# Kernel tuning notes

Hardware: AMD Instinct MI355X
Metric: run time of the kernel (lower is better)

Reference implementation:

```python
import jax, jax.numpy as jnp
import numpy as np
import math

E = 3        # e_layers
D = 512      # d_model
H = 8        # n_heads
FACTOR = 5
NEG = -1e9   # large-negative stand-in for -inf causal mask (same softmax result, NaN-safe)


def _layernorm(x, g, b, eps=1e-5):
    mu = jnp.mean(x, -1, keepdims=True)
    xc = x - mu
    var = jnp.mean(xc * xc, -1, keepdims=True)
    return g * xc * jax.lax.rsqrt(var + eps) + b


def _conv1d(x, w, b, pad):
    # x: [B,C,L], w: [O,I,K]
    y = jax.lax.conv_general_dilated(x, w, (1,), [pad], dimension_numbers=('NCH', 'OIH', 'NCH'))
    return y + b[None, :, None]


def _maxpool3s2(x):
    # x: [B,C,L] -> kernel 3, stride 2, pad 1
    return jax.lax.reduce_window(x, -jnp.inf, jax.lax.max, (1, 1, 3), (1, 1, 2), [(0, 0), (0, 0), (1, 1)])


def _prob_sparse(h, mask, wq, bq, wk, bk, wv, bv, wo, bo, key):
    B, L, Dm = h.shape
    hd = Dm // H
    scale = hd ** -0.5
    split = lambda y: y.reshape(B, L, H, hd).transpose(0, 2, 1, 3)  # [B,H,L,hd]
    Q = split(h @ wq + bq)
    K = split(h @ wk + bk)
    V = split(h @ wv + bv)
    U = FACTOR * int(math.ceil(math.log(L)))
    u = min(U, L)
    sample_k = min(U, L)
    perm = jax.random.permutation(key, L)[:sample_k]
    K_sample = K[:, :, perm, :]                                     # [B,H,sk,hd]
    qks = jnp.einsum('bhld,bhsd->bhls', Q, K_sample) * scale        # [B,H,L,sk]
    M = qks.max(-1) - qks.mean(-1)                                  # sparsity measure [B,H,L]
    _, idx = jax.lax.top_k(M, u)                                    # [B,H,u]
    Q_reduce = jnp.take_along_axis(Q, idx[..., None], axis=2)       # [B,H,u,hd]
    logits = jnp.einsum('bhud,bhld->bhul', Q_reduce, K) * scale + mask[idx]  # [B,H,u,L]
    attn = jax.nn.softmax(logits, -1)
    out_reduce = jnp.einsum('bhul,bhld->bhud', attn, V)             # [B,H,u,hd]
    out = jnp.broadcast_to(V.mean(axis=2, keepdims=True), (B, H, L, hd))
    out = out.at[jnp.arange(B)[:, None, None], jnp.arange(H)[None, :, None], idx].set(out_reduce)
    return out.transpose(0, 2, 1, 3).reshape(B, L, Dm) @ wo + bo


def setup_inputs() -> dict:
    key = jax.random.key(0)
    it = iter(jax.random.split(key, 64))
    nrm = lambda *sh: jax.random.normal(next(it), sh, jnp.float32) * 0.02
    B, L, IN = 8, 4096, 64
    inp = {}
    inp['x'] = jax.random.normal(next(it), (B, L, IN), jnp.float32)
    inp['time_features'] = jax.random.normal(next(it), (B, L, 2), jnp.float32)
    inp['in_w'] = nrm(IN, D)
    inp['in_b'] = jnp.zeros((D,), jnp.float32)
    inp['pos_emb'] = nrm(1, L, D)
    inp['tp_w'] = nrm(2, D)
    inp['tp_b'] = jnp.zeros((D,), jnp.float32)
    inp['pos_scale'] = jnp.ones((1,), jnp.float32)
    inp['temporal_scale'] = jnp.ones((1,), jnp.float32)
    inp['conv_w'] = nrm(E, D, D, 3)
    inp['conv_b'] = jnp.zeros((E, D), jnp.float32)
    for nm in ('wq', 'wk', 'wv', 'wo'):
        inp[nm] = nrm(E, D, D)
    for nm in ('bq', 'bk', 'bv', 'bo'):
        inp[nm] = jnp.zeros((E, D), jnp.float32)
    inp['f1_w'] = nrm(E, D, 4 * D)
    inp['f1_b'] = jnp.zeros((E, 4 * D), jnp.float32)
    inp['f2_w'] = nrm(E, 4 * D, D)
    inp['f2_b'] = jnp.zeros((E, D), jnp.float32)
    for nm in ('g1', 'g2', 'g3'):
        inp[nm] = jnp.ones((E, D), jnp.float32)
    for nm in ('be1', 'be2', 'be3'):
        inp[nm] = jnp.zeros((E, D), jnp.float32)
    inp['dconv_w'] = nrm(E - 1, D, D, 3)
    inp['dconv_b'] = jnp.zeros((E - 1, D), jnp.float32)
    return inp


def reference(x, time_features, in_w, in_b, pos_emb, tp_w, tp_b, pos_scale, temporal_scale,
              conv_w, conv_b, wq, bq, wk, bk, wv, bv, wo, bo,
              f1_w, f1_b, f2_w, f2_b, g1, be1, g2, be2, g3, be3, dconv_w, dconv_b):
    B, L, _ = x.shape
    h = x @ in_w + in_b + pos_scale * pos_emb[:, :L] + temporal_scale * (time_features @ tp_w + tp_b)
    for i in range(E):
        Lc = h.shape[1]
        mask = jnp.triu(jnp.full((Lc, Lc), NEG, h.dtype), k=1)
        # causal conv: left-pad 2, kernel 3
        c = _conv1d(h.transpose(0, 2, 1), conv_w[i], conv_b[i], (2, 0)).transpose(0, 2, 1)
        h = _layernorm(h + c, g1[i], be1[i])
        a = _prob_sparse(h, mask, wq[i], bq[i], wk[i], bk[i], wv[i], bv[i], wo[i], bo[i],
                         jax.random.fold_in(jax.random.key(42), i))
        h = _layernorm(h + a, g2[i], be2[i])
        f = jax.nn.relu(h @ f1_w[i] + f1_b[i]) @ f2_w[i] + f2_b[i]
        h = _layernorm(h + f, g3[i], be3[i])
        if i < E - 1:
            hc = _conv1d(h.transpose(0, 2, 1), dconv_w[i], dconv_b[i], (1, 1))
            h = _maxpool3s2(jax.nn.elu(hc)).transpose(0, 2, 1)
    return h
```

## Files before the change

kernel.cpp:

```cpp
#include <hip/hip_runtime.h>
#include <cstdint>
#include <cmath>
#include <cstddef>

#define DD 512
#define NEGV -1000000000.0f
#define MAXU 45

typedef unsigned short ushort_t;
typedef __attribute__((ext_vector_type(8))) short short8v;
typedef __attribute__((ext_vector_type(4))) float float4v;

__device__ __forceinline__ ushort_t bfbits(float x) {
  uint32_t u = __float_as_uint(x);
  return (ushort_t)((u + 0x7FFFu + ((u >> 16) & 1u)) >> 16);
}
__device__ __forceinline__ float bfval(ushort_t b) {
  return __uint_as_float(((uint32_t)b) << 16);
}
__device__ __forceinline__ void split3(float x, ushort_t& o0, ushort_t& o1, ushort_t& o2) {
  ushort_t b0 = bfbits(x); float f0 = bfval(b0);
  float r1 = x - f0;       ushort_t b1 = bfbits(r1); float f1 = bfval(b1);
  float r2 = r1 - f1;      o2 = bfbits(r2);
  o0 = b0; o1 = b1;
}

__device__ __forceinline__ void d_tf(uint32_t k0, uint32_t k1,
                                     uint32_t c0, uint32_t c1,
                                     uint32_t& o0, uint32_t& o1) {
  const uint32_t ks2 = k0 ^ k1 ^ 0x1BD11BDAu;
  uint32_t v0 = c0 + k0, v1 = c1 + k1;
#define RR(r) { v0 += v1; v1 = (v1 << r) | (v1 >> (32 - r)); v1 ^= v0; }
  RR(13) RR(15) RR(26) RR(6)  v0 += k1;  v1 += ks2 + 1u;
  RR(17) RR(29) RR(16) RR(24) v0 += ks2; v1 += k0 + 2u;
  RR(13) RR(15) RR(26) RR(6)  v0 += k0;  v1 += k1 + 3u;
  RR(17) RR(29) RR(16) RR(24) v0 += k1;  v1 += ks2 + 4u;
  RR(13) RR(15) RR(26) RR(6)  v0 += ks2; v1 += k0 + 5u;
#undef RR
  o0 = v0; o1 = v1;
}

__device__ __forceinline__ uint32_t bits_elem(int B, uint32_t k0, uint32_t k1,
                                              uint32_t i, uint32_t total) {
  uint32_t a, b;
  switch (B) {
    case 0: case 1: {
      const uint32_t half = total >> 1;
      if (i < half) { d_tf(k0, k1, i, i + half, a, b); return B == 0 ? a : b; }
      d_tf(k0, k1, i - half, i, a, b); return B == 0 ? b : a;
    }
    case 2: d_tf(k0, k1, 0u, i, a, b); return a;
    case 3: d_tf(k0, k1, 0u, i, a, b); return b;
    case 4: d_tf(k0, k1, 0u, i, a, b); return a ^ b;
    case 5: d_tf(k0, k1, i, 0u, a, b); return a;
    case 6: d_tf(k0, k1, i, 0u, a, b); return b;
    default: d_tf(k0, k1, i, 0u, a, b); return a ^ b;
  }
}

__device__ __forceinline__ void split_row2(int S, int B, uint32_t k0, uint32_t k1,
                                           int num, int row,
                                           uint32_t& o0, uint32_t& o1) {
  uint32_t a, b;
  switch (S) {
    case 0: case 2: {
      const bool sw = (S == 2);
      const int m0 = 2 * row, m1 = 2 * row + 1;
      if (m0 < num) { d_tf(k0, k1, (uint32_t)m0, (uint32_t)(m0 + num), a, b); o0 = sw ? b : a; }
      else          { d_tf(k0, k1, (uint32_t)(m0 - num), (uint32_t)m0, a, b); o0 = sw ? a : b; }
      if (m1 < num) { d_tf(k0, k1, (uint32_t)m1, (uint32_t)(m1 + num), a, b); o1 = sw ? b : a; }
      else          { d_tf(k0, k1, (uint32_t)(m1 - num), (uint32_t)m1, a, b); o1 = sw ? a : b; }
      return;
    }
    case 1: {
      if (B >= 5) d_tf(k0, k1, (uint32_t)row, 0u, o0, o1);
      else        d_tf(k0, k1, 0u, (uint32_t)row, o0, o1);
      return;
    }
    default: {
      const uint32_t p0 = 2 * row, p1 = 2 * row + 1;
      uint32_t x0, x1, y0, y1;
      if (B >= 5) { d_tf(k0, k1, p0, 0u, x0, x1); d_tf(k0, k1, p1, 0u, y0, y1); }
      else        { d_tf(k0, k1, 0u, p0, x0, x1); d_tf(k0, k1, 0u, p1, y0, y1); }
      if (S == 3)      { o0 = x0;      o1 = y0; }
      else if (S == 4) { o0 = x1;      o1 = y1; }
      else             { o0 = x0 ^ x1; o1 = y0 ^ y1; }
      return;
    }
  }
}

__global__ __launch_bounds__(64) void probe_k(const float* __restrict__ x,
                                              int* __restrict__ flag) {
  const int t = threadIdx.x;
  const float val_ref = erff(x[t] * 0.70710678118654752f);
  const float lo = __uint_as_float(0xBF7FFFFFu);
  const float span = 1.0f - lo;
  int match = -1;
  for (int S = 0; S < 6; ++S) {
    for (int B = 0; B < 8; ++B) {
      uint32_t xk0, xk1;
      split_row2(S, B, 0u, 0u, 64, 0, xk0, xk1);
      const uint32_t bits = bits_elem(B, xk0, xk1, (uint32_t)t, 1u << 21);
      const float u = __uint_as_float((bits >> 9) | 0x3F800000u) - 1.0f;
      const float val = fmaxf(lo, u * span + lo);
      const unsigned long long m = __ballot(fabsf(val - val_ref) < 2e-2f);
      if (match < 0 && __popcll(m) >= 58) match = S * 8 + B;
    }
  }
  uint32_t s00, s01, s10, s11;
  split_row2(0, 0, 0u, 0u, 2, 0, s00, s01);
  split_row2(0, 0, 0u, 0u, 2, 1, s10, s11);
  const int self_ok = (s00 == 4146024105u && s01 == 967050713u &&
                       s10 == 2718843009u && s11 == 1272950319u) ? 1 : 0;
  if (t == 0) { flag[0] = match; flag[1] = self_ok; }
}

__global__ __launch_bounds__(1024) void perm_k(const int* __restrict__ flag,
                                               int* __restrict__ permout,
                                               int L, int U, int layer) {
  __shared__ unsigned long long comp[4096];
  __shared__ int xs[4096];
  const int tid = threadIdx.x;
  int c = flag[0]; if (c < 0) c = 0;
  const int S = c >> 3, B = c & 7;
  uint32_t k0, k1;
  d_tf(0u, 42u, 0u, (uint32_t)layer, k0, k1);
  const int rounds = (L >= 2048) ? 2 : 1;
  for (int i = tid; i < L; i += 1024) xs[i] = i;
  __syncthreads();
  for (int r = 0; r < rounds; ++r) {
    uint32_t nk0, nk1, sk0, sk1;
    split_row2(S, B, k0, k1, 2, 0, nk0, nk1);
    split_row2(S, B, k0, k1, 2, 1, sk0, sk1);
    k0 = nk0; k1 = nk1;
    for (int i = tid; i < L; i += 1024) {
      const uint32_t bits = bits_elem(B, sk0, sk1, (uint32_t)i, (uint32_t)L);
      comp[i] = ((unsigned long long)bits << 32) | (unsigned)i;
    }
    __syncthreads();
    for (int kk = 2; kk <= L; kk <<= 1) {
      for (int jj = kk >> 1; jj > 0; jj >>= 1) {
        for (int t2 = tid; t2 < (L >> 1); t2 += 1024) {
          const int i = ((t2 & ~(jj - 1)) << 1) | (t2 & (jj - 1));
          const int ixj = i | jj;
          const bool asc = ((i & kk) == 0);
          const unsigned long long a = comp[i], b = comp[ixj];
          if ((a > b) == asc) { comp[i] = b; comp[ixj] = a; }
        }
        __syncthreads();
      }
    }
    int vals[4]; int n = 0;
    for (int i = tid; i < L; i += 1024) vals[n++] = xs[comp[i] & 0xFFFFFFFFu];
    __syncthreads();
    n = 0;
    for (int i = tid; i < L; i += 1024) xs[i] = vals[n++];
    __syncthreads();
  }
  for (int i = tid; i < U; i += 1024) permout[i] = xs[i];
}

__global__ void diag_k(const int* __restrict__ flag, float* __restrict__ out) {
  if (threadIdx.x == 0 && blockIdx.x == 0 && flag[0] < 0)
    out[0] = flag[1] ? 54321.0f : 94321.0f;
}

__global__ void zero_pads_k(ushort_t* __restrict__ A0, ushort_t* __restrict__ A1,
                            ushort_t* __restrict__ A2, int PR, int total) {
  const int i = blockIdx.x * 256 + threadIdx.x;
  if (i >= total) return;
  const int bl = i / 1536;
  const int rem = i - bl * 1536;
  const int pj = rem >> 9, c = rem & 511;
  const int j = (pj < 2) ? pj : (PR - 1);
  const size_t o = ((size_t)bl * PR + j) * 512 + c;
  A0[o] = 0; A1[o] = 0; A2[o] = 0;
}

__global__ __launch_bounds__(256) void embed_split_k(
    const float* __restrict__ x, const float* __restrict__ tfe,
    const float* __restrict__ in_w, const float* __restrict__ in_b,
    const float* __restrict__ pos_emb, const float* __restrict__ tp_w,
    const float* __restrict__ tp_b, const float* __restrict__ ps,
    const float* __restrict__ ts, ushort_t* __restrict__ A0,
    ushort_t* __restrict__ A1, ushort_t* __restrict__ A2,
    int L, int lcs, int PR) {
  const int r = blockIdx.x;
  const int l = r & (L - 1);
  const int bl = r >> lcs;
  __shared__ float xs[64];
  __shared__ float tfs[2];
  const int t = threadIdx.x;
  if (t < 64) xs[t] = x[(size_t)r * 64 + t];
  if (t < 2)  tfs[t] = tfe[(size_t)r * 2 + t];
  __syncthreads();
  const float p = ps[0], tsc = ts[0];
  const size_t ob = ((size_t)bl * PR + 2 + l) * 512;
  for (int c = t; c < DD; c += 256) {
    float s = in_b[c];
#pragma unroll 8
    for (int k = 0; k < 64; ++k) s = fmaf(xs[k], in_w[k * DD + c], s);
    float tv = tfs[0] * tp_w[c] + tfs[1] * tp_w[DD + c] + tp_b[c];
    const float v = s + p * pos_emb[(size_t)l * DD + c] + tsc * tv;
    ushort_t u0, u1, u2; split3(v, u0, u1, u2);
    A0[ob + c] = u0; A1[ob + c] = u1; A2[ob + c] = u2;
  }
}

__global__ void wsplit_k(const float* __restrict__ W, ushort_t* __restrict__ B0,
                         ushort_t* __restrict__ B1, ushort_t* __restrict__ B2,
                         int K, int N, int conv, int total) {
  const int i = blockIdx.x * 256 + threadIdx.x;
  if (i >= total) return;
  const int n = i / K, k = i - n * K;
  const float v = conv ? W[(size_t)n * 1536 + (k & 511) * 3 + (k >> 9)]
                       : W[(size_t)k * N + n];
  ushort_t u0, u1, u2; split3(v, u0, u1, u2);
  B0[i] = u0; B1[i] = u1; B2[i] = u2;
}

__global__ void cat2_k(const float* __restrict__ a, const float* __restrict__ b,
                       float* __restrict__ o) {
  const int i = blockIdx.x * 256 + threadIdx.x;
  if (i < 512) o[i] = a[i];
  else if (i < 1024) o[i] = b[i - 512];
}

__global__ void asm_split_k(const int* __restrict__ map, const float* __restrict__ outred,
                            const float* __restrict__ vm, ushort_t* __restrict__ A0,
                            ushort_t* __restrict__ A1, ushort_t* __restrict__ A2,
                            int U, int Lc, int lcs, int PR, int bc, long total) {
  const long i = (long)blockIdx.x * 256 + threadIdx.x;
  if (i >= total) return;
  const int c = (int)(i & 511);
  const long r = i >> 9;
  const int bl = (int)(r >> lcs);
  const int t = (int)(r & (Lc - 1));
  const int b = bc + bl;
  const int head = c >> 6, d = c & 63;
  const int bh = b * 8 + head;
  const int j = map[(size_t)bh * Lc + t];
  const float v = (j >= 0) ? outred[((size_t)(bh * U + j) << 6) + d]
                           : vm[(bh << 6) + d];
  ushort_t u0, u1, u2; split3(v, u0, u1, u2);
  const size_t o = ((size_t)bl * PR + 2 + t) * 512 + c;
  A0[o] = u0; A1[o] = u1; A2[o] = u2;
}

template <int MH, int NW>
__global__ __launch_bounds__(256, (MH + NW <= 2) ? 4 : ((MH == 1) ? 4 : 3))
void gemm6_k(
    const ushort_t* __restrict__ A0, const ushort_t* __restrict__ A1,
    const ushort_t* __restrict__ A2, const ushort_t* __restrict__ B0,
    const ushort_t* __restrict__ B1, const ushort_t* __restrict__ B2,
    float* __restrict__ C, float* __restrict__ C2,
    ushort_t* __restrict__ Co0, ushort_t* __restrict__ Co1,
    ushort_t* __restrict__ Co2, const float* __restrict__ bias,
    int N, int K, int RS, int PR, int Foff, int lcs, int rowoff, int relu,
    int mode, int conv3, int p3) {
  __shared__ ushort_t sm[6144 * MH + 6144 * NW];
  const int tid = threadIdx.x;
  const int nwg = gridDim.x * gridDim.y;
  const int bid0 = blockIdx.y * gridDim.x + blockIdx.x;
  const int wgid = ((bid0 & 7) * (nwg >> 3)) + (bid0 >> 3);
  const int bn = (wgid % gridDim.x) * (64 * NW);
  const int bm = (wgid / gridDim.x) * (64 * MH);
  const int lane = tid & 63;
  const int w = tid >> 6;
  const int wn = w * (16 * NW);
  const int l15 = lane & 15;
  const int c16r = lane >> 4;
  const int Lcm = (1 << lcs) - 1;
  float4v acc[MH][4][NW] = {};

  const int NCH = 3 * MH + 3 * NW;
  const ushort_t* gp[NCH];
  int lb[NCH];
  int isl2[NCH];
  {
    const int rowc = lane >> 2;
    const int slot = lane & 3;
#pragma unroll
    for (int j = 0; j < NCH; ++j) {
      const int q = w + 4 * j;
      if (q < 12 * MH) {
        const int limb = q / (4 * MH), ql = q % (4 * MH);
        const int rl = ql * 16 + rowc;
        const int dcol = slot ^ ((rl >> 1) & 3);
        const int r = rowoff + bm + rl;
        const int b = r >> lcs, t = r & Lcm;
        const size_t off = ((size_t)(b * PR + Foff + t)) * RS + dcol * 8;
        gp[j] = (limb == 0 ? A0 : limb == 1 ? A1 : A2) + off;
        isl2[j] = (limb == 2);
      } else {
        const int qq = q - 12 * MH;
        const int limb = qq / (4 * NW), ql = qq % (4 * NW);
        const int rl = ql * 16 + rowc;
        const int dcol = slot ^ ((rl >> 1) & 3);
        const size_t off = ((size_t)(bn + rl)) * K + dcol * 8;
        gp[j] = (limb == 0 ? B0 : limb == 1 ? B1 : B2) + off;
        isl2[j] = (limb == 2);
      }
      lb[j] = q * 512;
    }
  }

  const int ABASE1 = 2048 * MH, ABASE2 = 4096 * MH;
  const int BBASE = 6144 * MH;
  const int BL = 2048 * NW;
  const int nsteps = K >> 5;
  for (int s = 0; s < nsteps; ++s) {
    const int k0 = conv3 ? ((s % 3) * 512 + (s / 3) * 32) : (s * 32);
#pragma unroll
    for (int j = 0; j < NCH; ++j) {
      if (p3 && isl2[j]) continue;
      __builtin_amdgcn_global_load_lds(
          (const __attribute__((address_space(1))) void*)(gp[j] + k0),
          (__attribute__((address_space(3))) void*)(sm + lb[j]),
          16, 0, 0);
    }
    __syncthreads();
    short8v bg0[NW], bg1[NW], bg2[NW];
#pragma unroll
    for (int g = 0; g < NW; ++g) {
      const int r = wn + g * 16 + l15;
      const int br = r * 32 + ((c16r ^ ((r >> 1) & 3)) << 3);
      bg0[g] = *(const short8v*)(sm + BBASE + br);
      bg1[g] = *(const short8v*)(sm + BBASE + BL + br);
      if (!p3) bg2[g] = *(const short8v*)(sm + BBASE + 2 * BL + br);
    }
#pragma unroll
    for (int h = 0; h < MH; ++h) {
#pragma unroll
      for (int mf = 0; mf < 4; ++mf) {
        const int r = h * 64 + mf * 16 + l15;
        const int ar = r * 32 + ((c16r ^ ((r >> 1) & 3)) << 3);
        const short8v a0 = *(const short8v*)(sm + ar);
        const short8v a1 = *(const short8v*)(sm + ABASE1 + ar);
#pragma unroll
        for (int nf = 0; nf < NW; ++nf) {
          float4v c = acc[h][mf][nf];
          c = __builtin_amdgcn_mfma_f32_16x16x32_bf16(a0, bg0[nf], c, 0, 0, 0);
          c = __builtin_amdgcn_mfma_f32_16x16x32_bf16(a0, bg1[nf], c, 0, 0, 0);
          c = __builtin_amdgcn_mfma_f32_16x16x32_bf16(a1, bg0[nf], c, 0, 0, 0);
          acc[h][mf][nf] = c;
        }
        if (!p3) {
          const short8v a2 = *(const short8v*)(sm + ABASE2 + ar);
#pragma unroll
          for (int nf = 0; nf < NW; ++nf) {
            float4v c = acc[h][mf][nf];
            c = __builtin_amdgcn_mfma_f32_16x16x32_bf16(a1, bg1[nf], c, 0, 0, 0);
            c = __builtin_amdgcn_mfma_f32_16x16x32_bf16(a0, bg2[nf], c, 0, 0, 0);
            c = __builtin_amdgcn_mfma_f32_16x16x32_bf16(a2, bg0[nf], c, 0, 0, 0);
            acc[h][mf][nf] = c;
          }
        }
      }
    }
    __syncthreads();
  }
  const int cbase = bn + wn + l15;
#pragma unroll
  for (int h = 0; h < MH; ++h) {
    const int rbase = bm + h * 64 + ((lane >> 4) << 2);
#pragma unroll
    for (int mf = 0; mf < 4; ++mf)
#pragma unroll
      for (int nf = 0; nf < NW; ++nf)
#pragma unroll
        for (int j = 0; j < 4; ++j) {
          const int row = rbase + mf * 16 + j;
          const int col = cbase + nf * 16;
          float v = acc[h][mf][nf][j] + bias[col];
          if (relu) v = fmaxf(v, 0.f);
          if (mode == 0) {
            C[(size_t)row * N + col] = v;
          } else if (mode == 1) {
            ushort_t u0, u1, u2; split3(v, u0, u1, u2);
            const size_t o = (size_t)row * N + col;
            Co0[o] = u0; Co1[o] = u1; Co2[o] = u2;
          } else {
            float* dst = (col >> 9) ? C2 : C;
            dst[(size_t)row * 512 + (col & 511)] = v;
          }
        }
  }
}

__global__ __launch_bounds__(64) void resid_ln_split_k(
    const ushort_t* __restrict__ A0, const ushort_t* __restrict__ A1,
    const ushort_t* __restrict__ A2, const float* __restrict__ res,
    const float* __restrict__ g, const float* __restrict__ be,
    ushort_t* __restrict__ O0, ushort_t* __restrict__ O1,
    ushort_t* __restrict__ O2, float* __restrict__ fout,
    int Lc, int lcs, int PR, int final_out) {
  const int r = blockIdx.x;
  const int t = threadIdx.x;
  const size_t lbase = (((size_t)(r >> lcs)) * PR + 2 + (r & (Lc - 1))) * 512 + t * 8;
  const short8v l0 = *(const short8v*)(A0 + lbase);
  const short8v l1 = *(const short8v*)(A1 + lbase);
  const short8v l2 = *(const short8v*)(A2 + lbase);
  const float4* rp = (const float4*)(res + (size_t)r * DD + t * 8);
  const float4 r0 = rp[0], r1 = rp[1];
  float h[8];
#pragma unroll
  for (int j = 0; j < 8; ++j)
    h[j] = bfval((ushort_t)l0[j]) + bfval((ushort_t)l1[j]) + bfval((ushort_t)l2[j]);
  h[0] += r0.x; h[1] += r0.y; h[2] += r0.z; h[3] += r0.w;
  h[4] += r1.x; h[5] += r1.y; h[6] += r1.z; h[7] += r1.w;
  float s = 0.f, q = 0.f;
#pragma unroll
  for (int j = 0; j < 8; ++j) { s += h[j]; q += h[j] * h[j]; }
  for (int off = 32; off; off >>= 1) { s += __shfl_down(s, off); q += __shfl_down(q, off); }
  s = __shfl(s, 0); q = __shfl(q, 0);
  const float mu = s * (1.f / 512.f);
  const float var = q * (1.f / 512.f) - mu * mu;
  const float rs = rsqrtf(var + 1e-5f);
  const int c0 = t * 8;
  if (final_out) {
    float o[8];
#pragma unroll
    for (int j = 0; j < 8; ++j)
      o[j] = g[c0 + j] * (h[j] - mu) * rs + be[c0 + j];
    float4* op = (float4*)(fout + (size_t)r * DD + c0);
    op[0] = make_float4(o[0], o[1], o[2], o[3]);
    op[1] = make_float4(o[4], o[5], o[6], o[7]);
  } else {
    short8v o0, o1v, o2;
#pragma unroll
    for (int j = 0; j < 8; ++j) {
      const float v = g[c0 + j] * (h[j] - mu) * rs + be[c0 + j];
      ushort_t u0, u1, u2; split3(v, u0, u1, u2);
      o0[j] = (short)u0; o1v[j] = (short)u1; o2[j] = (short)u2;
    }
    *(short8v*)(O0 + lbase) = o0;
    *(short8v*)(O1 + lbase) = o1v;
    *(short8v*)(O2 + lbase) = o2;
  }
}

__global__ __launch_bounds__(256) void sample_m3_k(
    const float* __restrict__ Q, const float* __restrict__ Kb,
    float* __restrict__ Mv, const int* __restrict__ perm,
    int U, int Lc, int lcs) {
  const int tile = blockIdx.x;
  const int bh = blockIdx.y;
  const int head = bh & 7, b = bh >> 3;
  const int t = threadIdx.x;
  __shared__ float ks[MAXU][65];
  for (int e = t; e < U * 64; e += 256) {
    const int j = e >> 6, d = e & 63;
    ks[j][d] = Kb[(((size_t)b << lcs) + perm[j]) * DD + head * 64 + d];
  }
  __syncthreads();
  const int l = tile * 256 + t;
  const float4* qr = (const float4*)(Q + (((size_t)b << lcs) + l) * DD + head * 64);
  float q[64];
#pragma unroll
  for (int d4 = 0; d4 < 16; ++d4) {
    const float4 v = qr[d4];
    q[d4 * 4] = v.x; q[d4 * 4 + 1] = v.y; q[d4 * 4 + 2] = v.z; q[d4 * 4 + 3] = v.w;
  }
  float smax = -1e30f, ssum = 0.f;
  for (int j = 0; j < U; ++j) {
    float s = 0.f;
#pragma unroll
    for (int d = 0; d < 64; ++d) s = fmaf(q[d], ks[j][d], s);
    smax = fmaxf(smax, s); ssum += s;
  }
  Mv[(size_t)bh * Lc + l] = 0.125f * (smax - ssum / (float)U);
}

__global__ __launch_bounds__(256) void topk_k(
    const float* __restrict__ Mv, int* __restrict__ idx, int Lc, int U) {
  __shared__ float mv[4096];
  __shared__ float rv[256];
  __shared__ int ri[256];
  const int bh = blockIdx.x;
  const int t = threadIdx.x;
  const float* Mp = Mv + (size_t)bh * Lc;
  for (int i = t; i < Lc; i += 256) mv[i] = Mp[i];
  __syncthreads();
  for (int j = 0; j < U; ++j) {
    float best = -INFINITY; int bi = 0x7fffffff;
    for (int i = t; i < Lc; i += 256) {
      const float v = mv[i];
      if (v > best) { best = v; bi = i; }
    }
    rv[t] = best; ri[t] = bi;
    __syncthreads();
    for (int s2 = 128; s2; s2 >>= 1) {
      if (t < s2) {
        if (rv[t + s2] > rv[t] || (rv[t + s2] == rv[t] && ri[t + s2] < ri[t])) {
          rv[t] = rv[t + s2]; ri[t] = ri[t + s2];
        }
      }
      __syncthreads();
    }
    if (t == 0) { idx[bh * U + j] = ri[0]; mv[ri[0]] = -INFINITY; }
    __syncthreads();
  }
}

__global__ void gather_q_k(const float* __restrict__ Q, const int* __restrict__ idx,
                           float* __restrict__ Qsel, int U, int Lc, int lc_shift,
                           int total) {
  const int i = blockIdx.x * 256 + threadIdx.x;
  if (i >= total) return;
  const int d = i & 63;
  const int gj = i >> 6;
  const int bh = gj / U;
  const int head = bh & 7, b = bh >> 3;
  const int qi = idx[gj];
  Qsel[i] = Q[(((size_t)b << lc_shift) + qi) * DD + head * 64 + d];
}

__global__ __launch_bounds__(256, 4) void attn_flash_k(
    const float* __restrict__ Qsel, const float* __restrict__ Kb,
    const float* __restrict__ V, const int* __restrict__ idx,
    float* __restrict__ Oseg, float* __restrict__ mseg, float* __restrict__ lseg,
    int U, int Lc, int lcs, int SEG) {
  const int seg = blockIdx.x;
  const int bh = blockIdx.y;
  const int head = bh & 7, b = bh >> 3;
  const int t = threadIdx.x;
  __shared__ float q[48][65];
  __shared__ float kt[32][65];
  __shared__ float vt[32][65];
  __shared__ float ps[48][33];
  __shared__ float mArr[48], lArr[48], fArr[48];
  __shared__ int qiArr[48];
  __shared__ int qmaxs;
#pragma unroll
  for (int i = 0; i < 12; ++i) {
    const int e = i * 256 + t;
    q[e >> 6][e & 63] = (e < U * 64) ? Qsel[(size_t)bh * U * 64 + e] : 0.f;
  }
  if (t < 48) {
    qiArr[t] = (t < U) ? idx[bh * U + t] : -1;
    mArr[t] = -1e30f; lArr[t] = 0.f; fArr[t] = 1.f;
  }
  if (t == 0) {
    int qm = 0;
    for (int j = 0; j < U; ++j) qm = max(qm, idx[bh * U + j]);
    qmaxs = qm;
  }
  float acc[12];
#pragma unroll
  for (int i = 0; i < 12; ++i) acc[i] = 0.f;
  __syncthreads();
  const int segl = Lc / SEG;
  const int s0 = seg * segl, s1 = s0 + segl;
  const int qmax = qmaxs;
  const size_t kvbase = ((size_t)b << lcs) * DD + head * 64;
  for (int t0 = s0; t0 < s1; t0 += 32) {
    if (t0 > qmax) break;
#pragma unroll
    for (int i = 0; i < 2; ++i) {
      const int idx4 = t + 256 * i;
      const int r = idx4 >> 4;
      const int c4 = (idx4 & 15) << 2;
      const float4 kv = *(const float4*)(Kb + kvbase + (size_t)(t0 + r) * DD + c4);
      const float4 vv = *(const float4*)(V + kvbase + (size_t)(t0 + r) * DD + c4);
      kt[r][c4] = kv.x; kt[r][c4 + 1] = kv.y; kt[r][c4 + 2] = kv.z; kt[r][c4 + 3] = kv.w;
      vt[r][c4] = vv.x; vt[r][c4 + 1] = vv.y; vt[r][c4 + 2] = vv.z; vt[r][c4 + 3] = vv.w;
    }
    __syncthreads();
#pragma unroll
    for (int i = 0; i < 6; ++i) {
      const int pair = i * 256 + t;
      const int qq = pair >> 5, l = pair & 31;
      const float* qr = q[qq];
      const float* kr = kt[l];
      float s = 0.f;
#pragma unroll
      for (int d = 0; d < 64; ++d) s = fmaf(qr[d], kr[d], s);
      s *= 0.125f;
      if (t0 + l > qiArr[qq]) s = NEGV;
      ps[qq][l] = s;
    }
    __syncthreads();
    if (t < U) {
      float mrow = -1e30f;
      for (int l = 0; l < 32; ++l) mrow = fmaxf(mrow, ps[t][l]);
      const float mnew = fmaxf(mArr[t], mrow);
      const float f = expf(mArr[t] - mnew);
      float sum = 0.f;
      for (int l = 0; l < 32; ++l) {
        const float e = expf(ps[t][l] - mnew);
        ps[t][l] = e; sum += e;
      }
      lArr[t] = lArr[t] * f + sum;
      mArr[t] = mnew; fArr[t] = f;
    }
    __syncthreads();
#pragma unroll
    for (int i = 0; i < 12; ++i) {
      const int pair = i * 256 + t;
      const int qq = pair >> 6, d = pair & 63;
      float a = acc[i] * fArr[qq];
      const float* pr = ps[qq];
#pragma unroll
      for (int l = 0; l < 32; ++l) a = fmaf(pr[l], vt[l][d], a);
      acc[i] = a;
    }
    __syncthreads();
  }
  const size_t obase = ((size_t)(bh * SEG + seg)) * U * 64;
#pragma unroll
  for (int i = 0; i < 12; ++i) {
    const int pair = i * 256 + t;
    if (pair < U * 64) Oseg[obase + pair] = acc[i];
  }
  if (t < U) {
    mseg[(bh * SEG + seg) * U + t] = mArr[t];
    lseg[(bh * SEG + seg) * U + t] = lArr[t];
  }
}

__global__ void attn_comb_k(const float* __restrict__ Oseg,
                            const float* __restrict__ mseg,
                            const float* __restrict__ lseg,
                            float* __restrict__ outred, int U, int SEG) {
  const int bh = blockIdx.x;
  const int t = threadIdx.x;
  for (int i = 0; i < 12; ++i) {
    const int pair = i * 256 + t;
    if (pair >= U * 64) break;
    const int qq = pair >> 6;
    float m = -1e30f;
    for (int s = 0; s < SEG; ++s) m = fmaxf(m, mseg[(bh * SEG + s) * U + qq]);
    float l = 0.f, o = 0.f;
    for (int s = 0; s < SEG; ++s) {
      const float w = expf(mseg[(bh * SEG + s) * U + qq] - m);
      l += w * lseg[(bh * SEG + s) * U + qq];
      o += w * Oseg[((size_t)(bh * SEG + s)) * U * 64 + pair];
    }
    outred[(size_t)bh * U * 64 + pair] = o / l;
  }
}

__global__ __launch_bounds__(256) void vmean1_k(
    const float* __restrict__ V, float* __restrict__ vpart, int Lc, int lcs) {
  const int seg = blockIdx.x;
  const int bh = blockIdx.y;
  const int head = bh & 7, b = bh >> 3;
  const int t = threadIdx.x;
  const int d = t & 63, c = t >> 6;
  const int segl = Lc >> 4;
  const int l0 = seg * segl;
  float s = 0.f;
  for (int l = l0 + c; l < l0 + segl; l += 4)
    s += V[(((size_t)b << lcs) + l) * DD + head * 64 + d];
  __shared__ float red[256];
  red[t] = s; __syncthreads();
  if (t < 64)
    vpart[((bh * 16 + seg) << 6) + t] = red[t] + red[64 + t] + red[128 + t] + red[192 + t];
}

__global__ void vmean2_k(const float* __restrict__ vpart, float* __restrict__ vm,
                         int Lc) {
  const int bh = blockIdx.x;
  const int d = threadIdx.x;
  float s = 0.f;
  for (int seg = 0; seg < 16; ++seg) s += vpart[((bh * 16 + seg) << 6) + d];
  vm[(bh << 6) + d] = s / (float)Lc;
}

__global__ void fill_i32_k(int* __restrict__ p, int n, int v) {
  const int i = blockIdx.x * 256 + threadIdx.x;
  if (i < n) p[i] = v;
}

__global__ void scatter_k(const int* __restrict__ idx, int* __restrict__ map,
                          int U, int Lc, int total) {
  const int i = blockIdx.x * 256 + threadIdx.x;
  if (i < total) map[(size_t)(i / U) * Lc + idx[i]] = i % U;
}

__global__ void elu_pool_split_k(const float* __restrict__ X,
                                 ushort_t* __restrict__ A0, ushort_t* __restrict__ A1,
                                 ushort_t* __restrict__ A2,
                                 int Lc, int lcs, int PRn, long total) {
  const long i = (long)blockIdx.x * 256 + threadIdx.x;
  if (i >= total) return;
  const int c = (int)(i & 511);
  const long r = i >> 9;
  const int half = Lc >> 1;
  const int t2 = (int)(r & (half - 1));
  const int bl = (int)(r >> (lcs - 1));
  float m = -INFINITY;
  const int t00 = 2 * t2 - 1;
  for (int dt = 0; dt < 3; ++dt) {
    const int tt = t00 + dt;
    if (tt >= 0 && tt < Lc) {
      float v = X[(((size_t)bl << lcs) + tt) * 512 + c];
      v = v > 0.f ? v : expm1f(v);
      m = fmaxf(m, v);
    }
  }
  ushort_t u0, u1, u2; split3(m, u0, u1, u2);
  const size_t o = ((size_t)bl * PRn + 2 + t2) * 512 + c;
  A0[o] = u0; A1[o] = u1; A2[o] = u2;
}

extern "C" void kernel_launch(void* const* d_in, const int* in_sizes, int n_in,
                              void* d_out, int out_size, void* d_ws, size_t ws_size,
                              hipStream_t stream) {
  (void)in_sizes; (void)n_in; (void)out_size;
  const float* x       = (const float*)d_in[0];
  const float* tfe     = (const float*)d_in[1];
  const float* in_w    = (const float*)d_in[2];
  const float* in_b    = (const float*)d_in[3];
  const float* pos_emb = (const float*)d_in[4];
  const float* tp_w    = (const float*)d_in[5];
  const float* tp_b    = (const float*)d_in[6];
  const float* pos_s   = (const float*)d_in[7];
  const float* tmp_s   = (const float*)d_in[8];
  const float* conv_w  = (const float*)d_in[9];
  const float* conv_b  = (const float*)d_in[10];
  const float* wq      = (const float*)d_in[11];
  const float* wk      = (const float*)d_in[12];
  const float* wv      = (const float*)d_in[13];
  const float* wo      = (const float*)d_in[14];
  const float* bq      = (const float*)d_in[15];
  const float* bk      = (const float*)d_in[16];
  const float* bv      = (const float*)d_in[17];
  const float* bo      = (const float*)d_in[18];
  const float* f1_w    = (const float*)d_in[19];
  const float* f1_b    = (const float*)d_in[20];
  const float* f2_w    = (const float*)d_in[21];
  const float* f2_b    = (const float*)d_in[22];
  const float* g1      = (const float*)d_in[23];
  const float* g2      = (const float*)d_in[24];
  const float* g3      = (const float*)d_in[25];
  const float* be1     = (const float*)d_in[26];
  const float* be2     = (const float*)d_in[27];
  const float* be3     = (const float*)d_in[28];
  const float* dconv_w = (const float*)d_in[29];
  const float* dconv_b = (const float*)d_in[30];

  const size_t SZ = 16777216;
  const size_t HSF = 16789504;
  const size_t WSZ = 1048576;
  const size_t CSZ = 8400896;
  float* ws    = (float*)d_ws;
  float* slotB = ws;
  float* slotC = ws + SZ;
  ushort_t* hA0 = (ushort_t*)(ws + 2 * SZ);
  ushort_t* hA1 = hA0 + HSF;
  ushort_t* hA2 = hA1 + HSF;
  ushort_t* w10 = hA2 + HSF; ushort_t* w11 = w10 + WSZ; ushort_t* w12 = w11 + WSZ;
  ushort_t* w20 = w12 + WSZ; ushort_t* w21 = w20 + WSZ; ushort_t* w22 = w21 + WSZ;
  float* Mb    = (float*)(w22 + WSZ);
  float* ORb   = Mb + 262144;
  float* VMb   = ORb + 196608;
  int*   idxb  = (int*)(VMb + 8192);
  int*   mapb  = idxb + 8192;
  int*   flagb = mapb + 262144;
  int*   permb = flagb + 64;
  float* Qselb = (float*)(permb + 64);
  float* bcatb = Qselb + 196608;
  float* vpartb = bcatb + 1024;
  float* Osegb = vpartb + 65536;
  float* msegb = Osegb + 2949120;
  float* lsegb = msegb + 46080;
  const size_t NEED = (size_t)((char*)(lsegb + 46080) - (char*)ws);
  if (ws_size < NEED) return;

  ushort_t* cs0 = (ushort_t*)slotC;
  ushort_t* cs1 = cs0 + CSZ;
  ushort_t* cs2 = cs1 + CSZ;
  ushort_t* fc0 = (ushort_t*)slotC;
  ushort_t* fc1 = fc0 + (size_t)4096 * 2048;
  ushort_t* fc2 = fc1 + (size_t)4096 * 2048;

  probe_k<<<1, 64, 0, stream>>>(x, flagb);

  int L = 4096;
  {
    int lcs = 12;
    const int PR = L + 3;
    embed_split_k<<<8 * L, 256, 0, stream>>>(x, tfe, in_w, in_b, pos_emb, tp_w,
                                             tp_b, pos_s, tmp_s, hA0, hA1, hA2,
                                             L, lcs, PR);
    zero_pads_k<<<(8 * 3 * 512 + 255) / 256, 256, 0, stream>>>(hA0, hA1, hA2,
                                                               PR, 8 * 3 * 512);
  }

  for (int i = 0; i < 3; ++i) {
    const int Lc = L;
    int lcs = 0; while ((1 << lcs) < Lc) ++lcs;
    const int R = 8 * Lc;
    const int U = (Lc == 4096) ? 45 : (Lc == 2048 ? 40 : 35);
    const int PR = Lc + 3;
    const int SEG = (Lc == 4096) ? 16 : (Lc == 2048 ? 8 : 4);
    const int p3 = (i == 2);
    const dim3 gfull2(4, R / 128);

    perm_k<<<1, 1024, 0, stream>>>(flagb, permb, Lc, U, i);

    wsplit_k<<<3072, 256, 0, stream>>>(conv_w + (size_t)i * 786432, w10, w11, w12,
                                       1536, 512, 1, 786432);
    gemm6_k<2, 2><<<gfull2, 256, 0, stream>>>(hA0, hA1, hA2, w10, w11, w12,
        slotB, nullptr, nullptr, nullptr, nullptr,
        conv_b + i * 512, 512, 1536, 512, PR, 0, lcs, 0, 0, 0, 1, 0);
    resid_ln_split_k<<<R, 64, 0, stream>>>(hA0, hA1, hA2, slotB,
        g1 + i * 512, be1 + i * 512, hA0, hA1, hA2, nullptr, Lc, lcs, PR, 0);

    cat2_k<<<4, 256, 0, stream>>>(bq + i * 512, bk + i * 512, bcatb);
    wsplit_k<<<1024, 256, 0, stream>>>(wq + (size_t)i * 262144, w10, w11, w12,
                                       512, 512, 0, 262144);
    wsplit_k<<<1024, 256, 0, stream>>>(wk + (size_t)i * 262144, w10 + 262144,
                                       w11 + 262144, w12 + 262144, 512, 512, 0, 262144);
    wsplit_k<<<1024, 256, 0, stream>>>(wv + (size_t)i * 262144, w20, w21, w22,
                                       512, 512, 0, 262144);
    gemm6_k<2, 2><<<dim3(8, R / 128), 256, 0, stream>>>(hA0, hA1, hA2, w10, w11, w12,
        slotC, slotB, nullptr, nullptr, nullptr, bcatb,
        1024, 512, 512, PR, 2, lcs, 0, 0, 2, 0, 0);
    sample_m3_k<<<dim3(Lc / 256, 64), 256, 0, stream>>>(slotC, slotB, Mb, permb,
                                                        U, Lc, lcs);
    topk_k<<<64, 256, 0, stream>>>(Mb, idxb, Lc, U);
    gather_q_k<<<(64 * U * 64 + 255) / 256, 256, 0, stream>>>(slotC, idxb, Qselb,
                                                              U, Lc, lcs, 64 * U * 64);
    gemm6_k<2, 2><<<gfull2, 256, 0, stream>>>(hA0, hA1, hA2, w20, w21, w22,
        slotC, nullptr, nullptr, nullptr, nullptr,
        bv + i * 512, 512, 512, 512, PR, 2, lcs, 0, 0, 0, 0, p3);

    attn_flash_k<<<dim3(SEG, 64), 256, 0, stream>>>(Qselb, slotB, slotC, idxb,
                                                    Osegb, msegb, lsegb, U, Lc, lcs, SEG);
    attn_comb_k<<<64, 256, 0, stream>>>(Osegb, msegb, lsegb, ORb, U, SEG);
    vmean1_k<<<dim3(16, 64), 256, 0, stream>>>(slotC, vpartb, Lc, lcs);
    vmean2_k<<<64, 64, 0, stream>>>(vpartb, VMb, Lc);
    fill_i32_k<<<(64 * Lc + 255) / 256, 256, 0, stream>>>(mapb, 64 * Lc, -1);
    scatter_k<<<(64 * U + 255) / 256, 256, 0, stream>>>(idxb, mapb, U, Lc, 64 * U);
    wsplit_k<<<1024, 256, 0, stream>>>(wo + (size_t)i * 262144, w10, w11, w12,
                                       512, 512, 0, 262144);
    {
      const int NBg = (Lc == 4096) ? 4 : 8;
      const int nchw = 8 / NBg;
      const long atotw = (long)NBg * Lc * 512;
      for (int ch = 0; ch < nchw; ++ch) {
        const int bc = ch * NBg;
        asm_split_k<<<(unsigned)((atotw + 255) / 256), 256, 0, stream>>>(
            mapb, ORb, VMb, cs0, cs1, cs2, U, Lc, lcs, PR, bc, atotw);
        gemm6_k<2, 2><<<dim3(4, (NBg * Lc) / 128), 256, 0, stream>>>(
            cs0, cs1, cs2, w10, w11, w12,
            slotB + (size_t)bc * Lc * 512, nullptr, nullptr, nullptr, nullptr,
            bo + i * 512, 512, 512, 512, PR, 2, lcs, 0, 0, 0, 0, p3);
      }
    }
    resid_ln_split_k<<<R, 64, 0, stream>>>(hA0, hA1, hA2, slotB,
        g2 + i * 512, be2 + i * 512, hA0, hA1, hA2, nullptr, Lc, lcs, PR, 0);

    wsplit_k<<<4096, 256, 0, stream>>>(f1_w + (size_t)i * 1048576, w10, w11, w12,
                                       512, 2048, 0, 1048576);
    wsplit_k<<<4096, 256, 0, stream>>>(f2_w + (size_t)i * 1048576, w20, w21, w22,
                                       2048, 512, 0, 1048576);
    for (int rc = 0; rc < R; rc += 4096) {
      for (int nh = 0; nh < 2; ++nh) {
        const int nc0 = nh * 1024;
        gemm6_k<1, 2><<<dim3(8, 64), 256, 0, stream>>>(hA0, hA1, hA2,
            w10 + (size_t)nc0 * 512, w11 + (size_t)nc0 * 512, w12 + (size_t)nc0 * 512,
            nullptr, nullptr, fc0 + nc0, fc1 + nc0, fc2 + nc0, f1_b + i * 2048 + nc0,
            2048, 512, 512, PR, 2, lcs, rc, 1, 1, 0, p3);
      }
      gemm6_k<1, 1><<<dim3(8, 64), 256, 0, stream>>>(fc0, fc1, fc2, w20, w21, w22,
          slotB + (size_t)rc * 512, nullptr, nullptr, nullptr, nullptr,
          f2_b + i * 512, 512, 2048, 2048, 4096, 0, 12, 0, 0, 0, 0, p3);
    }
    const int fin = (i == 2);
    resid_ln_split_k<<<R, 64, 0, stream>>>(hA0, hA1, hA2, slotB,
        g3 + i * 512, be3 + i * 512, hA0, hA1, hA2, (float*)d_out, Lc, lcs, PR, fin);

    if (i < 2) {
      wsplit_k<<<3072, 256, 0, stream>>>(dconv_w + (size_t)i * 786432, w10, w11, w12,
                                         1536, 512, 1, 786432);
      gemm6_k<2, 2><<<gfull2, 256, 0, stream>>>(hA0, hA1, hA2, w10, w11, w12,
          slotB, nullptr, nullptr, nullptr, nullptr,
          dconv_b + i * 512, 512, 1536, 512, PR, 1, lcs, 0, 0, 0, 1, 0);
      const int PRn = Lc / 2 + 3;
      elu_pool_split_k<<<(unsigned)(((long)8 * (Lc / 2) * 512) / 256), 256, 0, stream>>>(
          slotB, hA0, hA1, hA2, Lc, lcs, PRn, (long)8 * (Lc / 2) * 512);
      zero_pads_k<<<(8 * 3 * 512 + 255) / 256, 256, 0, stream>>>(hA0, hA1, hA2,
                                                                 PRn, 8 * 3 * 512);
      L = Lc / 2;
    }
  }

  diag_k<<<1, 64, 0, stream>>>(flagb, (float*)d_out);
}
```

Before: 5.196 ms.

## Replace dense output projection with mean-row projection plus sparse delta corrections

Most attention output rows equal the per-head V mean, so the output projection is rewritten as vm@wo+bo computed once per batch, plus rank-64 corrections only for the heads whose row was selected by top-k. This drops the full split-bf16 assembly and the dense 3-pass GEMM over all rows, along with its weight split. The new per-row kernel is fp32 CUDA-core work and, when rows have many selected heads, can be slower per row than the tensor-core GEMM.

After: 5.128 ms. Within noise of the previous version (-1.3%).

```diff
diff --git a/kernel.cpp b/kernel.cpp
--- a/kernel.cpp
+++ b/kernel.cpp
@@ -227,27 +227,6 @@
   else if (i < 1024) o[i] = b[i - 512];
 }
 
-__global__ void asm_split_k(const int* __restrict__ map, const float* __restrict__ outred,
-                            const float* __restrict__ vm, ushort_t* __restrict__ A0,
-                            ushort_t* __restrict__ A1, ushort_t* __restrict__ A2,
-                            int U, int Lc, int lcs, int PR, int bc, long total) {
-  const long i = (long)blockIdx.x * 256 + threadIdx.x;
-  if (i >= total) return;
-  const int c = (int)(i & 511);
-  const long r = i >> 9;
-  const int bl = (int)(r >> lcs);
-  const int t = (int)(r & (Lc - 1));
-  const int b = bc + bl;
-  const int head = c >> 6, d = c & 63;
-  const int bh = b * 8 + head;
-  const int j = map[(size_t)bh * Lc + t];
-  const float v = (j >= 0) ? outred[((size_t)(bh * U + j) << 6) + d]
-                           : vm[(bh << 6) + d];
-  ushort_t u0, u1, u2; split3(v, u0, u1, u2);
-  const size_t o = ((size_t)bl * PR + 2 + t) * 512 + c;
-  A0[o] = u0; A1[o] = u1; A2[o] = u2;
-}
-
 template <int MH, int NW>
 __global__ __launch_bounds__(256, (MH + NW <= 2) ? 4 : ((MH == 1) ? 4 : 3))
 void gemm6_k(
@@ -678,6 +657,54 @@
                           int U, int Lc, int total) {
   const int i = blockIdx.x * 256 + threadIdx.x;
   if (i < total) map[(size_t)(i / U) * Lc + idx[i]] = i % U;
+}
+
+__global__ __launch_bounds__(512) void vmw_k(const float* __restrict__ vm,
+                                             const float* __restrict__ wo,
+                                             const float* __restrict__ bo,
+                                             float* __restrict__ vmw) {
+  const int b = blockIdx.x;
+  const int c = threadIdx.x;
+  __shared__ float v[512];
+  v[c] = vm[(b * 8 + (c >> 6)) * 64 + (c & 63)];
+  __syncthreads();
+  float s = bo[c];
+  for (int k = 0; k < 512; ++k) s = fmaf(v[k], wo[k * 512 + c], s);
+  vmw[b * 512 + c] = s;
+}
+
+__global__ __launch_bounds__(256) void wo_delta_k(
+    const int* __restrict__ map, const float* __restrict__ outred,
+    const float* __restrict__ vm, const float* __restrict__ vmw,
+    const float* __restrict__ wo, float* __restrict__ out,
+    int U, int Lc, int lcs) {
+  const int r = blockIdx.x;
+  const int b = r >> lcs, t = r & (Lc - 1);
+  const int tid = threadIdx.x;
+  __shared__ float delta[64];
+  __shared__ int js[8];
+  if (tid < 8) js[tid] = map[((size_t)(b * 8 + tid)) * Lc + t];
+  __syncthreads();
+  float s0 = vmw[b * 512 + tid];
+  float s1 = vmw[b * 512 + tid + 256];
+  for (int h = 0; h < 8; ++h) {
+    const int j = js[h];
+    if (j < 0) continue;
+    const int bh = b * 8 + h;
+    if (tid < 64)
+      delta[tid] = outred[((size_t)(bh * U + j) << 6) + tid] - vm[(bh << 6) + tid];
+    __syncthreads();
+    const int base = h * 64;
+#pragma unroll 8
+    for (int d = 0; d < 64; ++d) {
+      const float dv = delta[d];
+      s0 = fmaf(dv, wo[(size_t)(base + d) * 512 + tid], s0);
+      s1 = fmaf(dv, wo[(size_t)(base + d) * 512 + tid + 256], s1);
+    }
+    __syncthreads();
+  }
+  out[(size_t)r * 512 + tid] = s0;
+  out[(size_t)r * 512 + tid + 256] = s1;
 }
 
 __global__ void elu_pool_split_k(const float* __restrict__ X,
@@ -745,7 +772,6 @@
   const size_t SZ = 16777216;
   const size_t HSF = 16789504;
   const size_t WSZ = 1048576;
-  const size_t CSZ = 8400896;
   float* ws    = (float*)d_ws;
   float* slotB = ws;
   float* slotC = ws + SZ;
@@ -767,12 +793,10 @@
   float* Osegb = vpartb + 65536;
   float* msegb = Osegb + 2949120;
   float* lsegb = msegb + 46080;
-  const size_t NEED = (size_t)((char*)(lsegb + 46080) - (char*)ws);
+  float* vmwb  = lsegb + 46080;
+  const size_t NEED = (size_t)((char*)(vmwb + 4096) - (char*)ws);
   if (ws_size < NEED) return;
 
-  ushort_t* cs0 = (ushort_t*)slotC;
-  ushort_t* cs1 = cs0 + CSZ;
-  ushort_t* cs2 = cs1 + CSZ;
   ushort_t* fc0 = (ushort_t*)slotC;
   ushort_t* fc1 = fc0 + (size_t)4096 * 2048;
   ushort_t* fc2 = fc1 + (size_t)4096 * 2048;
@@ -836,22 +860,9 @@
     vmean2_k<<<64, 64, 0, stream>>>(vpartb, VMb, Lc);
     fill_i32_k<<<(64 * Lc + 255) / 256, 256, 0, stream>>>(mapb, 64 * Lc, -1);
     scatter_k<<<(64 * U + 255) / 256, 256, 0, stream>>>(idxb, mapb, U, Lc, 64 * U);
-    wsplit_k<<<1024, 256, 0, stream>>>(wo + (size_t)i * 262144, w10, w11, w12,
-                                       512, 512, 0, 262144);
-    {
-      const int NBg = (Lc == 4096) ? 4 : 8;
-      const int nchw = 8 / NBg;
-      const long atotw = (long)NBg * Lc * 512;
-      for (int ch = 0; ch < nchw; ++ch) {
-        const int bc = ch * NBg;
-        asm_split_k<<<(unsigned)((atotw + 255) / 256), 256, 0, stream>>>(
-            mapb, ORb, VMb, cs0, cs1, cs2, U, Lc, lcs, PR, bc, atotw);
-        gemm6_k<2, 2><<<dim3(4, (NBg * Lc) / 128), 256, 0, stream>>>(
-            cs0, cs1, cs2, w10, w11, w12,
-            slotB + (size_t)bc * Lc * 512, nullptr, nullptr, nullptr, nullptr,
-            bo + i * 512, 512, 512, 512, PR, 2, lcs, 0, 0, 0, 0, p3);
-      }
-    }
+    vmw_k<<<8, 512, 0, stream>>>(VMb, wo + (size_t)i * 262144, bo + i * 512, vmwb);
+    wo_delta_k<<<R, 256, 0, stream>>>(mapb, ORb, VMb, vmwb,
+                                      wo + (size_t)i * 262144, slotB, U, Lc, lcs);
     resid_ln_split_k<<<R, 64, 0, stream>>>(hA0, hA1, hA2, slotB,
         g2 + i * 512, be2 + i * 512, hA0, hA1, hA2, nullptr, Lc, lcs, PR, 0);
 
```
